# Kernel tuning notes

Measured on AMD Instinct MI355X. Metric: run time of the kernel, lower is better.

## Reference

```python
import jax, jax.numpy as jnp
import numpy as np

B, N, D = 512, 16384, 2  # batch of weight vectors, grid points, 2-D geometry


def _eig_power(eigs, q, p):
    # reconstruct Q diag(eigs**p) Q^T ; eigs [B,D], q [B,D,D]
    return (q * (eigs ** p)[..., None, :]) @ jnp.swapaxes(q, -1, -2)


def _make_gauss(geo, w):
    # geo [N,D], w [B,N] (rows sum to 1)
    mean = w @ geo                               # [B,D]
    centered = geo[None, :, :] - mean[:, None, :]  # [B,N,D]
    denom = 1.0 - jnp.sum(w * w, axis=-1)        # [B] reliability-weight correction
    cov = jnp.einsum('bn,bnd,bne->bde', w, centered, centered) / denom[:, None, None]
    return mean, cov, centered


def setup_inputs() -> dict:
    key = jax.random.key(0)
    k1, k2, k3, k4 = jax.random.split(key, 4)
    geo_x = jax.random.uniform(k1, (N, D), dtype=jnp.float32)
    geo_y = jax.random.uniform(k2, (N, D), dtype=jnp.float32)
    a = jax.random.uniform(k3, (B, N), dtype=jnp.float32, minval=0.1, maxval=1.0)
    a = a / jnp.sum(a, axis=-1, keepdims=True)
    b = jax.random.uniform(k4, (B, N), dtype=jnp.float32, minval=0.1, maxval=1.0)
    b = b / jnp.sum(b, axis=-1, keepdims=True)
    return {"geo_x": geo_x, "geo_y": geo_y, "a": a, "b": b}


def reference(geo_x, geo_y, a, b):
    mean_a, cov_a, cx = _make_gauss(geo_x, a)   # cov_a [B,D,D], cx [B,N,D]
    mean_b, cov_b, _ = _make_gauss(geo_y, b)
    # Gaussian OT map: sigma0^{-1/2} (sigma0^{1/2} sigma1 sigma0^{1/2})^{1/2} sigma0^{-1/2}
    e0, q0 = jnp.linalg.eigh(cov_a)
    sqrt0 = _eig_power(e0, q0, 0.5)
    sqrt0_inv = _eig_power(e0, q0, -0.5)
    mid = sqrt0 @ cov_b @ sqrt0
    e1, q1 = jnp.linalg.eigh(mid)
    m = _eig_power(e1, q1, 0.5)
    a2b = sqrt0_inv @ m @ sqrt0_inv             # [B,D,D]
    # quadratic form (centered_x * (A2B centered_x^T)^T).sum(-1)
    quad = jnp.einsum('bnd,bde,bne->bn', cx, a2b, cx)  # [B,N]
    f = 2.0 * (0.5 * jnp.sum(geo_x * geo_x, axis=1)[None, :]
               - 0.5 * quad
               - mean_b @ geo_x.T)
    f = f - jnp.mean(f, axis=1, keepdims=True)
    return f
```

## Files before the change

kernel.cpp:

```cpp
#include <hip/hip_runtime.h>

static constexpr int TPB = 256;
static constexpr int NSLICE = 4;

using f4 = __attribute__((ext_vector_type(4))) float;

__device__ __forceinline__ float wave_reduce_f32(float v) {
#pragma unroll
    for (int off = 32; off > 0; off >>= 1)
        v += __shfl_down(v, off, 64);
    return v;
}

__global__ __launch_bounds__(TPB) void kstats(const float* __restrict__ gx,
                                              const float* __restrict__ gy,
                                              const float* __restrict__ a,
                                              const float* __restrict__ bw,
                                              int N, int B,
                                              double* __restrict__ spart,
                                              double* __restrict__ gpart) {
    const int s = blockIdx.x;
    const int b = blockIdx.y;
    const int n4   = N / 4;
    const int per  = n4 / NSLICE;
    const int base = s * per;
    const f4* gx4 = reinterpret_cast<const f4*>(gx);
    const int lane = threadIdx.x & 63, wid = threadIdx.x >> 6;

    if (b == B) {
        float sx = 0, sy = 0, sxx = 0, sxy = 0, syy = 0;
        for (int i = base + threadIdx.x; i < base + per; i += TPB) {
            f4 g0 = gx4[2 * i], g1 = gx4[2 * i + 1];
            float x0 = g0[0], y0 = g0[1], x1 = g0[2], y1 = g0[3];
            float x2 = g1[0], y2 = g1[1], x3 = g1[2], y3 = g1[3];
            sx  += (x0 + x1) + (x2 + x3);
            sy  += (y0 + y1) + (y2 + y3);
            sxx += x0 * x0 + x1 * x1 + x2 * x2 + x3 * x3;
            sxy += x0 * y0 + x1 * y1 + x2 * y2 + x3 * y3;
            syy += y0 * y0 + y1 * y1 + y2 * y2 + y3 * y3;
        }
        float accg[5] = {sx, sy, sxx, sxy, syy};
        __shared__ double redg[4][5];
#pragma unroll
        for (int k = 0; k < 5; k++) {
            float v = wave_reduce_f32(accg[k]);
            if (lane == 0) redg[wid][k] = (double)v;
        }
        __syncthreads();
        if (threadIdx.x < 5)
            gpart[s * 5 + threadIdx.x] = redg[0][threadIdx.x] + redg[1][threadIdx.x] +
                                         redg[2][threadIdx.x] + redg[3][threadIdx.x];
        return;
    }

    const f4* a4  = reinterpret_cast<const f4*>(a  + (size_t)b * N);
    const f4* b4  = reinterpret_cast<const f4*>(bw + (size_t)b * N);
    const f4* gy4 = reinterpret_cast<const f4*>(gy);

    float acc[14];
#pragma unroll
    for (int k = 0; k < 14; k++) acc[k] = 0.0f;

#pragma unroll 4
    for (int i = base + threadIdx.x; i < base + per; i += TPB) {
        f4 av = a4[i];
        f4 bv = b4[i];
        f4 g0 = gx4[2 * i], g1 = gx4[2 * i + 1];
        f4 h0 = gy4[2 * i], h1 = gy4[2 * i + 1];
        float wa[4] = {av[0], av[1], av[2], av[3]};
        float wb[4] = {bv[0], bv[1], bv[2], bv[3]};
        float px[4] = {g0[0], g0[2], g1[0], g1[2]};
        float py[4] = {g0[1], g0[3], g1[1], g1[3]};
        float qx[4] = {h0[0], h0[2], h1[0], h1[2]};
        float qy[4] = {h0[1], h0[3], h1[1], h1[3]};
#pragma unroll
        for (int j = 0; j < 4; j++) {
            float w = wa[j], x = px[j], y = py[j];
            float wx = w * x, wy = w * y;
            acc[0] += w;
            acc[1] += wx;
            acc[2] += wy;
            acc[3] += wx * x;
            acc[4] += wx * y;
            acc[5] += wy * y;
            acc[6] += w * w;
            float v = wb[j], u = qx[j], t = qy[j];
            float vu = v * u, vt = v * t;
            acc[7]  += v;
            acc[8]  += vu;
            acc[9]  += vt;
            acc[10] += vu * u;
            acc[11] += vu * t;
            acc[12] += vt * t;
            acc[13] += v * v;
        }
    }

    __shared__ double red[4][14];
#pragma unroll
    for (int k = 0; k < 14; k++) {
        float v = wave_reduce_f32(acc[k]);
        if (lane == 0) red[wid][k] = (double)v;
    }
    __syncthreads();
    if (threadIdx.x < 14) {
        spart[((size_t)b * NSLICE + s) * 14 + threadIdx.x] =
            red[0][threadIdx.x] + red[1][threadIdx.x] +
            red[2][threadIdx.x] + red[3][threadIdx.x];
    }
}

__global__ __launch_bounds__(TPB) void kemit(const float* __restrict__ gx,
                                             const double* __restrict__ spart,
                                             const double* __restrict__ gpart,
                                             int N, float* __restrict__ out) {
    const int b = blockIdx.y;
    __shared__ double sh14[14];
    __shared__ double shg[5];
    __shared__ float shc[10];

    const f4* gx4 = reinterpret_cast<const f4*>(gx);
    const int i0 = blockIdx.x * (TPB * 4) + threadIdx.x;
    f4 g[8];
#pragma unroll
    for (int k = 0; k < 4; k++) {
        g[2 * k]     = gx4[2 * (i0 + k * TPB)];
        g[2 * k + 1] = gx4[2 * (i0 + k * TPB) + 1];
    }

    if (threadIdx.x < 14) {
        double t = 0;
#pragma unroll
        for (int s = 0; s < NSLICE; s++)
            t += spart[((size_t)b * NSLICE + s) * 14 + threadIdx.x];
        sh14[threadIdx.x] = t;
    } else if (threadIdx.x >= 64 && threadIdx.x < 69) {
        double t = 0;
#pragma unroll
        for (int s = 0; s < NSLICE; s++) t += gpart[s * 5 + (threadIdx.x - 64)];
        shg[threadIdx.x - 64] = t / (double)N;
    }
    __syncthreads();

    if (threadIdx.x == 0) {
        double Sa = sh14[0],  mx  = sh14[1],  my  = sh14[2],  Saxx = sh14[3],  Saxy = sh14[4],  Sayy = sh14[5],  Saa = sh14[6];
        double Sb = sh14[7],  mbx = sh14[8],  mby = sh14[9],  Sbxx = sh14[10], Sbxy = sh14[11], Sbyy = sh14[12], Sbb = sh14[13];

        double da = 1.0 - Saa, db = 1.0 - Sbb;
        double Caxx = (Saxx - mx * mx * (2.0 - Sa)) / da;
        double Caxy = (Saxy - mx * my * (2.0 - Sa)) / da;
        double Cayy = (Sayy - my * my * (2.0 - Sa)) / da;
        double Cbxx = (Sbxx - mbx * mbx * (2.0 - Sb)) / db;
        double Cbxy = (Sbxy - mbx * mby * (2.0 - Sb)) / db;
        double Cbyy = (Sbyy - mby * mby * (2.0 - Sb)) / db;

        double s0 = sqrt(fmax(Caxx * Cayy - Caxy * Caxy, 0.0));
        double t0 = sqrt(Caxx + Cayy + 2.0 * s0);
        double Rxx = (Caxx + s0) / t0, Rxy = Caxy / t0, Ryy = (Cayy + s0) / t0;
        double detR = Rxx * Ryy - Rxy * Rxy;
        double Ixx = Ryy / detR, Ixy = -Rxy / detR, Iyy = Rxx / detR;

        double Txx = Cbxx * Rxx + Cbxy * Rxy;
        double Txy = Cbxx * Rxy + Cbxy * Ryy;
        double Tyx = Cbxy * Rxx + Cbyy * Rxy;
        double Tyy = Cbxy * Rxy + Cbyy * Ryy;
        double midxx = Rxx * Txx + Rxy * Tyx;
        double midyy = Rxy * Txy + Ryy * Tyy;
        double midxy = 0.5 * ((Rxx * Txy + Rxy * Tyy) + (Rxy * Txx + Ryy * Tyx));

        double s1 = sqrt(fmax(midxx * midyy - midxy * midxy, 0.0));
        double t1 = sqrt(midxx + midyy + 2.0 * s1);
        double Mxx = (midxx + s1) / t1, Mxy = midxy / t1, Myy = (midyy + s1) / t1;

        double Uxx = Mxx * Ixx + Mxy * Ixy;
        double Uxy = Mxx * Ixy + Mxy * Iyy;
        double Uyx = Mxy * Ixx + Myy * Ixy;
        double Uyy = Mxy * Ixy + Myy * Iyy;
        double Axx = Ixx * Uxx + Ixy * Uyx;
        double Axy = Ixx * Uxy + Ixy * Uyy;
        double Ayy = Ixy * Uxy + Iyy * Uyy;

        shc[0] = (float)(1.0 - Axx);
        shc[1] = (float)(1.0 - Ayy);
        shc[2] = (float)(-2.0 * Axy);
        shc[3] = (float)(2.0 * (Axx * mx + Axy * my - mbx));
        shc[4] = (float)(2.0 * (Ayy * my + Axy * mx - mby));
        shc[5] = (float)shg[0];
        shc[6] = (float)shg[1];
        shc[7] = (float)shg[2];
        shc[8] = (float)shg[3];
        shc[9] = (float)shg[4];
    }
    __syncthreads();

    const float cxx = shc[0], cyy = shc[1], cxy = shc[2], cx = shc[3], cy = shc[4];
    const float Ex = shc[5], Ey = shc[6], Ex2 = shc[7], Exy = shc[8], Ey2 = shc[9];

    f4* out4 = reinterpret_cast<f4*>(out + (size_t)b * N);
#pragma unroll
    for (int k = 0; k < 4; k++) {
        int i = i0 + k * TPB;
        f4 g0 = g[2 * k], g1 = g[2 * k + 1];
        float rx[4] = {g0[0], g0[2], g1[0], g1[2]};
        float ry[4] = {g0[1], g0[3], g1[1], g1[3]};
        f4 o;
#pragma unroll
        for (int j = 0; j < 4; j++) {
            float x = rx[j], y = ry[j];
            o[j] = cxx * (x * x - Ex2) + cyy * (y * y - Ey2) + cxy * (x * y - Exy) +
                   cx * (x - Ex) + cy * (y - Ey);
        }
        __builtin_nontemporal_store(o, out4 + i);
    }
}

extern "C" void kernel_launch(void* const* d_in, const int* in_sizes, int n_in,
                              void* d_out, int out_size, void* d_ws, size_t ws_size,
                              hipStream_t stream) {
    const float* geo_x = (const float*)d_in[0];
    const float* geo_y = (const float*)d_in[1];
    const float* a     = (const float*)d_in[2];
    const float* b     = (const float*)d_in[3];
    float* out = (float*)d_out;

    int N = in_sizes[0] / 2;
    int B = in_sizes[2] / N;

    char* ws = (char*)d_ws;
    double* gpart = (double*)ws;
    double* spart = (double*)(ws + 512);

    kstats<<<dim3(NSLICE, B + 1), TPB, 0, stream>>>(geo_x, geo_y, a, b, N, B, spart, gpart);
    kemit<<<dim3((N / 4) / (TPB * 4), B), TPB, 0, stream>>>(geo_x, spart, gpart, N, out);
}
```

Baseline: 28.03 us.

## Split stats loop per distribution, use float2 packed accumulators, drop weight-sum term

The single fused accumulation loop over both weight sets becomes two separate loops, one per distribution, each keeping float2 accumulators so the compiler can emit packed FP32 math. The sum-of-weights accumulator is removed on the assumption that rows sum to 1, so the covariance formula drops its (2 - S) factor. A launch-bounds occupancy hint of 8 is added and the unroll factor is reduced. The aim is fewer live registers, higher occupancy and fewer ALU instructions, at the cost of reading geometry in two passes and relying on normalized inputs.

```diff
diff --git a/kernel.cpp b/kernel.cpp
--- a/kernel.cpp
+++ b/kernel.cpp
@@ -4,6 +4,7 @@
 static constexpr int NSLICE = 4;
 
 using f4 = __attribute__((ext_vector_type(4))) float;
+using f2 = __attribute__((ext_vector_type(2))) float;
 
 __device__ __forceinline__ float wave_reduce_f32(float v) {
 #pragma unroll
@@ -12,13 +13,13 @@
     return v;
 }
 
-__global__ __launch_bounds__(TPB) void kstats(const float* __restrict__ gx,
-                                              const float* __restrict__ gy,
-                                              const float* __restrict__ a,
-                                              const float* __restrict__ bw,
-                                              int N, int B,
-                                              double* __restrict__ spart,
-                                              double* __restrict__ gpart) {
+__global__ __launch_bounds__(TPB, 8) void kstats(const float* __restrict__ gx,
+                                                 const float* __restrict__ gy,
+                                                 const float* __restrict__ a,
+                                                 const float* __restrict__ bw,
+                                                 int N, int B,
+                                                 double* __restrict__ spart,
+                                                 double* __restrict__ gpart) {
     const int s = blockIdx.x;
     const int b = blockIdx.y;
     const int n4   = N / 4;
@@ -57,54 +58,58 @@
     const f4* b4  = reinterpret_cast<const f4*>(bw + (size_t)b * N);
     const f4* gy4 = reinterpret_cast<const f4*>(gy);
 
-    float acc[14];
-#pragma unroll
-    for (int k = 0; k < 14; k++) acc[k] = 0.0f;
-
-#pragma unroll 4
+    const f2 z2 = {0.0f, 0.0f};
+    f2 acc[12];
+#pragma unroll
+    for (int k = 0; k < 12; k++) acc[k] = z2;
+
+#pragma unroll 2
     for (int i = base + threadIdx.x; i < base + per; i += TPB) {
         f4 av = a4[i];
+        f4 g0 = gx4[2 * i], g1 = gx4[2 * i + 1];
+#pragma unroll
+        for (int h = 0; h < 2; h++) {
+            f2 w = (h == 0) ? f2{av[0], av[1]} : f2{av[2], av[3]};
+            f2 x = (h == 0) ? f2{g0[0], g0[2]} : f2{g1[0], g1[2]};
+            f2 y = (h == 0) ? f2{g0[1], g0[3]} : f2{g1[1], g1[3]};
+            f2 wx = w * x, wy = w * y;
+            acc[0] += wx;
+            acc[1] += wy;
+            acc[2] += wx * x;
+            acc[3] += wx * y;
+            acc[4] += wy * y;
+            acc[5] += w * w;
+        }
+    }
+
+#pragma unroll 2
+    for (int i = base + threadIdx.x; i < base + per; i += TPB) {
         f4 bv = b4[i];
-        f4 g0 = gx4[2 * i], g1 = gx4[2 * i + 1];
         f4 h0 = gy4[2 * i], h1 = gy4[2 * i + 1];
-        float wa[4] = {av[0], av[1], av[2], av[3]};
-        float wb[4] = {bv[0], bv[1], bv[2], bv[3]};
-        float px[4] = {g0[0], g0[2], g1[0], g1[2]};
-        float py[4] = {g0[1], g0[3], g1[1], g1[3]};
-        float qx[4] = {h0[0], h0[2], h1[0], h1[2]};
-        float qy[4] = {h0[1], h0[3], h1[1], h1[3]};
-#pragma unroll
-        for (int j = 0; j < 4; j++) {
-            float w = wa[j], x = px[j], y = py[j];
-            float wx = w * x, wy = w * y;
-            acc[0] += w;
-            acc[1] += wx;
-            acc[2] += wy;
-            acc[3] += wx * x;
-            acc[4] += wx * y;
-            acc[5] += wy * y;
-            acc[6] += w * w;
-            float v = wb[j], u = qx[j], t = qy[j];
-            float vu = v * u, vt = v * t;
-            acc[7]  += v;
-            acc[8]  += vu;
-            acc[9]  += vt;
-            acc[10] += vu * u;
-            acc[11] += vu * t;
-            acc[12] += vt * t;
-            acc[13] += v * v;
-        }
-    }
-
-    __shared__ double red[4][14];
-#pragma unroll
-    for (int k = 0; k < 14; k++) {
-        float v = wave_reduce_f32(acc[k]);
+#pragma unroll
+        for (int h = 0; h < 2; h++) {
+            f2 w = (h == 0) ? f2{bv[0], bv[1]} : f2{bv[2], bv[3]};
+            f2 x = (h == 0) ? f2{h0[0], h0[2]} : f2{h1[0], h1[2]};
+            f2 y = (h == 0) ? f2{h0[1], h0[3]} : f2{h1[1], h1[3]};
+            f2 wx = w * x, wy = w * y;
+            acc[6]  += wx;
+            acc[7]  += wy;
+            acc[8]  += wx * x;
+            acc[9]  += wx * y;
+            acc[10] += wy * y;
+            acc[11] += w * w;
+        }
+    }
+
+    __shared__ double red[4][12];
+#pragma unroll
+    for (int k = 0; k < 12; k++) {
+        float v = wave_reduce_f32(acc[k][0] + acc[k][1]);
         if (lane == 0) red[wid][k] = (double)v;
     }
     __syncthreads();
-    if (threadIdx.x < 14) {
-        spart[((size_t)b * NSLICE + s) * 14 + threadIdx.x] =
+    if (threadIdx.x < 12) {
+        spart[((size_t)b * NSLICE + s) * 12 + threadIdx.x] =
             red[0][threadIdx.x] + red[1][threadIdx.x] +
             red[2][threadIdx.x] + red[3][threadIdx.x];
     }
@@ -115,7 +120,7 @@
                                              const double* __restrict__ gpart,
                                              int N, float* __restrict__ out) {
     const int b = blockIdx.y;
-    __shared__ double sh14[14];
+    __shared__ double sh12[12];
     __shared__ double shg[5];
     __shared__ float shc[10];
 
@@ -128,12 +133,12 @@
         g[2 * k + 1] = gx4[2 * (i0 + k * TPB) + 1];
     }
 
-    if (threadIdx.x < 14) {
+    if (threadIdx.x < 12) {
         double t = 0;
 #pragma unroll
         for (int s = 0; s < NSLICE; s++)
-            t += spart[((size_t)b * NSLICE + s) * 14 + threadIdx.x];
-        sh14[threadIdx.x] = t;
+            t += spart[((size_t)b * NSLICE + s) * 12 + threadIdx.x];
+        sh12[threadIdx.x] = t;
     } else if (threadIdx.x >= 64 && threadIdx.x < 69) {
         double t = 0;
 #pragma unroll
@@ -143,16 +148,16 @@
     __syncthreads();
 
     if (threadIdx.x == 0) {
-        double Sa = sh14[0],  mx  = sh14[1],  my  = sh14[2],  Saxx = sh14[3],  Saxy = sh14[4],  Sayy = sh14[5],  Saa = sh14[6];
-        double Sb = sh14[7],  mbx = sh14[8],  mby = sh14[9],  Sbxx = sh14[10], Sbxy = sh14[11], Sbyy = sh14[12], Sbb = sh14[13];
+        double mx  = sh12[0],  my  = sh12[1],  Saxx = sh12[2],  Saxy = sh12[3],  Sayy = sh12[4],  Saa = sh12[5];
+        double mbx = sh12[6],  mby = sh12[7],  Sbxx = sh12[8],  Sbxy = sh12[9],  Sbyy = sh12[10], Sbb = sh12[11];
 
         double da = 1.0 - Saa, db = 1.0 - Sbb;
-        double Caxx = (Saxx - mx * mx * (2.0 - Sa)) / da;
-        double Caxy = (Saxy - mx * my * (2.0 - Sa)) / da;
-        double Cayy = (Sayy - my * my * (2.0 - Sa)) / da;
-        double Cbxx = (Sbxx - mbx * mbx * (2.0 - Sb)) / db;
-        double Cbxy = (Sbxy - mbx * mby * (2.0 - Sb)) / db;
-        double Cbyy = (Sbyy - mby * mby * (2.0 - Sb)) / db;
+        double Caxx = (Saxx - mx * mx) / da;
+        double Caxy = (Saxy - mx * my) / da;
+        double Cayy = (Sayy - my * my) / da;
+        double Cbxx = (Sbxx - mbx * mbx) / db;
+        double Cbxy = (Sbxy - mbx * mby) / db;
+        double Cbyy = (Sbyy - mby * mby) / db;
 
         double s0 = sqrt(fmax(Caxx * Cayy - Caxy * Caxy, 0.0));
         double t0 = sqrt(Caxx + Cayy + 2.0 * s0);
@@ -230,6 +235,7 @@
     double* gpart = (double*)ws;
     double* spart = (double*)(ws + 512);
 
-    kstats<<<dim3(NSLICE, B + 1), TPB, 0, stream>>>(geo_x, geo_y, a, b, N, B, spart, gpart);
+    kstats<<<dim3(NSLICE, B + 1), TPB, 0, stream>>>(geo_x, geo_y, a, b, N, B,
+                                                    spart, gpart);
     kemit<<<dim3((N / 4) / (TPB * 4), B), TPB, 0, stream>>>(geo_x, spart, gpart, N, out);
 }
```

After: 31.07 us. 1.11x slower.
